# Optimization experiments

Hardware: AMD Instinct MI355X
Metric: run time of the kernel (lower is better)

The kernel has to match this reference:

```python
import jax, jax.numpy as jnp
import numpy as np

DEPTH, HEADS, DH, DIM = 12, 12, 64, 768
SPARSITY = 0.5
EPS = 1e-5


def layernorm(x, g, b):
    mu = jnp.mean(x, axis=-1, keepdims=True)
    var = jnp.var(x, axis=-1, keepdims=True)
    return (x - mu) * jax.lax.rsqrt(var + EPS) * g + b


def ternary(W, sparsity):
    # TeTRA-style ternary quantization with magnitude-based sparsity:
    # drop the `sparsity` fraction of smallest-|w| weights, remaining -> sign(w)*mean|W|.
    a = jnp.abs(W)
    thr = jnp.quantile(a.ravel(), sparsity)
    scale = jnp.mean(a)
    return jnp.where(a >= thr, jnp.sign(W) * scale, jnp.zeros_like(W))


def setup_inputs() -> dict:
    key = jax.random.key(0)
    ks = jax.random.split(key, 10)
    w = lambda k, shape: jax.random.normal(k, shape, dtype=jnp.float32) * 0.02
    return {
        "img": jax.random.normal(ks[0], (32, 3, 224, 224), dtype=jnp.float32),
        "patch_ln_g": jnp.ones((768,), jnp.float32),
        "patch_ln_b": jnp.zeros((768,), jnp.float32),
        "W_patch": w(ks[1], (768, 768)),
        "b_patch": jnp.zeros((768,), jnp.float32),
        "emb_ln_g": jnp.ones((768,), jnp.float32),
        "emb_ln_b": jnp.zeros((768,), jnp.float32),
        "pos_emb": jax.random.normal(ks[2], (1, 197, 768), dtype=jnp.float32),
        "cls_token": jax.random.normal(ks[3], (1, 1, 768), dtype=jnp.float32),
        "ln1_g": jnp.ones((DEPTH, 768), jnp.float32),
        "ln1_b": jnp.zeros((DEPTH, 768), jnp.float32),
        "Wqkv": w(ks[4], (DEPTH, 768, 3 * HEADS * DH)),
        "b_qkv": jnp.zeros((DEPTH, 3 * HEADS * DH), jnp.float32),
        "Wo": w(ks[5], (DEPTH, HEADS * DH, 768)),
        "b_o": jnp.zeros((DEPTH, 768), jnp.float32),
        "ln2_g": jnp.ones((DEPTH, 768), jnp.float32),
        "ln2_b": jnp.zeros((DEPTH, 768), jnp.float32),
        "W1": w(ks[6], (DEPTH, 768, 3072)),
        "b1": jnp.zeros((DEPTH, 3072), jnp.float32),
        "W2": w(ks[7], (DEPTH, 3072, 768)),
        "b2": jnp.zeros((DEPTH, 768), jnp.float32),
        "norm_g": jnp.ones((768,), jnp.float32),
        "norm_b": jnp.zeros((768,), jnp.float32),
    }


def reference(img, patch_ln_g, patch_ln_b, W_patch, b_patch, emb_ln_g, emb_ln_b,
              pos_emb, cls_token, ln1_g, ln1_b, Wqkv, b_qkv, Wo, b_o,
              ln2_g, ln2_b, W1, b1, W2, b2, norm_g, norm_b):
    B = img.shape[0]
    P = 16
    # b c (h p1) (w p2) -> b (h w) (p1 p2 c)
    x = img.reshape(B, 3, 14, P, 14, P).transpose(0, 2, 4, 3, 5, 1).reshape(B, 196, P * P * 3)
    x = layernorm(x, patch_ln_g, patch_ln_b)
    x = x @ W_patch + b_patch
    x = layernorm(x, emb_ln_g, emb_ln_b)
    cls = jnp.broadcast_to(cls_token, (B, 1, DIM))
    x = jnp.concatenate([cls, x], axis=1) + pos_emb  # [B, 197, 768]

    scale = DH ** -0.5
    for i in range(DEPTH):
        # sparse-ternary attention
        h = layernorm(x, ln1_g[i], ln1_b[i])
        qkv = h @ ternary(Wqkv[i], SPARSITY) + b_qkv[i]
        q, k, v = jnp.split(qkv, 3, axis=-1)
        q = q.reshape(B, -1, HEADS, DH).transpose(0, 2, 1, 3)
        k = k.reshape(B, -1, HEADS, DH).transpose(0, 2, 1, 3)
        v = v.reshape(B, -1, HEADS, DH).transpose(0, 2, 1, 3)
        attn = jax.nn.softmax(jnp.einsum('bhid,bhjd->bhij', q, k) * scale, axis=-1)
        o = jnp.einsum('bhij,bhjd->bhid', attn, v).transpose(0, 2, 1, 3).reshape(B, -1, HEADS * DH)
        x = x + (o @ ternary(Wo[i], SPARSITY) + b_o[i])
        # feed-forward (last layer uses full-precision weights)
        h = layernorm(x, ln2_g[i], ln2_b[i])
        if i < DEPTH - 1:
            W1q, W2q = ternary(W1[i], SPARSITY), ternary(W2[i], SPARSITY)
        else:
            W1q, W2q = W1[i], W2[i]
        x = x + (jax.nn.gelu(h @ W1q + b1[i]) @ W2q + b2[i])

    return layernorm(x, norm_g, norm_b)
```

## Files before the change

kernel.cpp:

```cpp
#include <hip/hip_runtime.h>

typedef unsigned short ushort_t;
typedef unsigned int uint_t;
typedef float f32x4 __attribute__((ext_vector_type(4)));
typedef short bf16x8 __attribute__((ext_vector_type(8)));

#define B_ 32
#define T_ 197
#define M_ 6304
#define M0_ 6272
#define DEPTH_ 12
#define NMAT_ 46
#define HBINS_ 16384

#define X_OFF    0ULL
#define H_OFF    19365888ULL
#define QKVB_OFF 29048832ULL
#define O_OFF    58097664ULL
#define MID_OFF  67780608ULL
#define WT_OFF   106512384ULL
#define HIST_OFF 111230976ULL
#define H2_OFF   114245632ULL
#define SUMS_OFF 120274944ULL
#define SEL_OFF  120275200ULL
#define PAR_OFF  120276224ULL

__device__ __forceinline__ float b2f(ushort_t u) {
    return __uint_as_float(((uint_t)u) << 16);
}
__device__ __forceinline__ ushort_t f2b(float f) {
    uint_t u = __float_as_uint(f);
    u += 0x7FFFu + ((u >> 16) & 1u);
    return (ushort_t)(u >> 16);
}
__device__ __forceinline__ float gelu_f(float v) {
    float u = 0.7978845608028654f * (v + 0.044715f * v * v * v);
    return v / (1.f + __expf(-2.f * u));
}

__device__ __forceinline__ void gld_lds16(void* lds, const void* g) {
    __builtin_amdgcn_global_load_lds(
        (const __attribute__((address_space(1))) unsigned int*)g,
        (__attribute__((address_space(3))) unsigned int*)lds, 16, 0, 0);
}

__device__ __forceinline__ void mat_info(int m, const float* Wqkv, const float* Wo,
                                         const float* W1, const float* W2,
                                         const float** W, int* N) {
    if (m < 12)      { *W = Wqkv + (size_t)m * 1769472;        *N = 1769472; }
    else if (m < 24) { *W = Wo   + (size_t)(m - 12) * 589824;  *N = 589824; }
    else if (m < 35) { *W = W1   + (size_t)(m - 24) * 2359296; *N = 2359296; }
    else             { *W = W2   + (size_t)(m - 35) * 2359296; *N = 2359296; }
}
__device__ __forceinline__ int mat_n(int m) {
    if (m < 12) return 1769472;
    if (m < 24) return 589824;
    return 2359296;
}

__global__ __launch_bounds__(256) void hist1_kernel(const float* Wqkv, const float* Wo,
                                                    const float* W1, const float* W2,
                                                    uint_t* hist, float* sums) {
    __shared__ uint_t lh[HBINS_];
    int m = blockIdx.y;
    const float* W; int N;
    mat_info(m, Wqkv, Wo, W1, W2, &W, &N);
    int t = threadIdx.x;
    for (int i = t; i < HBINS_; i += 256) lh[i] = 0;
    __syncthreads();
    float s = 0.f;
    const float4* W4 = (const float4*)W;
    int ntile = N >> 12;
    for (int tb = blockIdx.x; tb < ntile; tb += gridDim.x) {
        const float4* p = W4 + (size_t)tb * 1024 + t;
        float4 w0 = p[0];
        float4 w1 = p[256];
        float4 w2 = p[512];
        float4 w3 = p[768];
        float vs[16] = { w0.x, w0.y, w0.z, w0.w, w1.x, w1.y, w1.z, w1.w,
                         w2.x, w2.y, w2.z, w2.w, w3.x, w3.y, w3.z, w3.w };
        #pragma unroll
        for (int q = 0; q < 16; q++) {
            uint_t ub = __float_as_uint(vs[q]) & 0x7FFFFFFFu;
            s += __uint_as_float(ub);
            uint_t bin = ub >> 17;
            if (bin > 16383u) bin = 16383u;
            atomicAdd(&lh[bin], 1u);
        }
    }
    __syncthreads();
    uint_t* gh = hist + (size_t)m * HBINS_;
    for (int i = t; i < HBINS_; i += 256)
        if (lh[i]) atomicAdd(&gh[i], lh[i]);
    for (int off = 32; off > 0; off >>= 1) s += __shfl_down(s, off, 64);
    if ((t & 63) == 0) atomicAdd(&sums[m], s);
}

__global__ __launch_bounds__(256) void sel1_kernel(const uint_t* hist, uint_t* sel) {
    int m = blockIdx.x, t = threadIdx.x;
    const uint_t* gh = hist + (size_t)m * HBINS_;
    int N = mat_n(m);
    uint_t own = 0;
    for (int i = 0; i < 64; i++) own += gh[t * 64 + i];
    __shared__ uint_t cs[256];
    cs[t] = own; __syncthreads();
    for (int o = 1; o < 256; o <<= 1) {
        uint_t vv = (t >= o) ? cs[t - o] : 0u;
        __syncthreads();
        cs[t] += vv;
        __syncthreads();
    }
    uint_t c = cs[t] - own;
    uint_t r1 = (uint_t)(N >> 1), r2 = r1 + 1;
    for (int i = 0; i < 64; i++) {
        uint_t hv = gh[t * 64 + i];
        if (hv) {
            uint_t bin = (uint_t)(t * 64 + i);
            if (r1 > c && r1 <= c + hv) { sel[m * 4 + 0] = bin; sel[m * 4 + 1] = c; }
            if (r2 > c && r2 <= c + hv) { sel[m * 4 + 2] = bin; sel[m * 4 + 3] = c; }
            c += hv;
        }
    }
}

__global__ __launch_bounds__(256) void hist2_kernel(const float* Wqkv, const float* Wo,
                                                    const float* W1, const float* W2,
                                                    const uint_t* sel, uint_t* h2) {
    int m = blockIdx.y;
    const float* W; int N;
    mat_info(m, Wqkv, Wo, W1, W2, &W, &N);
    uint_t b1 = sel[m * 4 + 0], b2 = sel[m * 4 + 2];
    uint_t* ha = h2 + (size_t)m * 2 * HBINS_;
    uint_t* hb = ha + HBINS_;
    int t = threadIdx.x;
    const float4* W4 = (const float4*)W;
    int ntile = N >> 12;
    for (int tb = blockIdx.x; tb < ntile; tb += gridDim.x) {
        const float4* p = W4 + (size_t)tb * 1024 + t;
        float4 w0 = p[0];
        float4 w1 = p[256];
        float4 w2 = p[512];
        float4 w3 = p[768];
        float vs[16] = { w0.x, w0.y, w0.z, w0.w, w1.x, w1.y, w1.z, w1.w,
                         w2.x, w2.y, w2.z, w2.w, w3.x, w3.y, w3.z, w3.w };
        #pragma unroll
        for (int q = 0; q < 16; q++) {
            uint_t ub = __float_as_uint(vs[q]) & 0x7FFFFFFFu;
            uint_t bin = ub >> 17;
            uint_t sub = (ub >> 3) & 0x3FFFu;
            if (bin == b1) atomicAdd(&ha[sub], 1u);
            if (bin == b2 && b2 != b1) atomicAdd(&hb[sub], 1u);
        }
    }
}

__global__ __launch_bounds__(256) void sel2_kernel(const uint_t* h2, const uint_t* sel,
                                                   const float* sums, float* par) {
    int m = blockIdx.x, t = threadIdx.x;
    int N = mat_n(m);
    uint_t b1 = sel[m * 4 + 0], below1 = sel[m * 4 + 1];
    uint_t b2 = sel[m * 4 + 2], below2 = sel[m * 4 + 3];
    const uint_t* ha = h2 + (size_t)m * 2 * HBINS_;
    const uint_t* hb = (b2 == b1) ? ha : ha + HBINS_;
    uint_t r1 = (uint_t)(N >> 1) - below1;
    uint_t r2 = (uint_t)(N >> 1) + 1 - below2;
    __shared__ uint_t cs[256];
    __shared__ uint_t subs[2];
    uint_t own = 0;
    for (int i = 0; i < 64; i++) own += ha[t * 64 + i];
    cs[t] = own; __syncthreads();
    for (int o = 1; o < 256; o <<= 1) {
        uint_t vv = (t >= o) ? cs[t - o] : 0u;
        __syncthreads(); cs[t] += vv; __syncthreads();
    }
    uint_t c = cs[t] - own;
    for (int i = 0; i < 64; i++) {
        uint_t hv = ha[t * 64 + i];
        if (hv) {
            if (r1 > c && r1 <= c + hv) subs[0] = (uint_t)(t * 64 + i);
            c += hv;
        }
    }
    __syncthreads();
    own = 0;
    for (int i = 0; i < 64; i++) own += hb[t * 64 + i];
    cs[t] = own; __syncthreads();
    for (int o = 1; o < 256; o <<= 1) {
        uint_t vv = (t >= o) ? cs[t - o] : 0u;
        __syncthreads(); cs[t] += vv; __syncthreads();
    }
    c = cs[t] - own;
    for (int i = 0; i < 64; i++) {
        uint_t hv = hb[t * 64 + i];
        if (hv) {
            if (r2 > c && r2 <= c + hv) subs[1] = (uint_t)(t * 64 + i);
            c += hv;
        }
    }
    __syncthreads();
    if (t == 0) {
        float v1 = __uint_as_float((b1 << 17) | (subs[0] << 3) | 4u);
        float v2 = __uint_as_float((b2 << 17) | (subs[1] << 3) | 4u);
        par[2 * m]     = 0.5f * (v1 + v2);
        par[2 * m + 1] = sums[m] / (float)N;
    }
}

__global__ __launch_bounds__(256) void trq_kernel(const float* W, ushort_t* Wt,
                                                  int K, int N, const float* params, int pidx) {
    __shared__ ushort_t tile[32][33];
    int n0 = blockIdx.x * 32, k0 = blockIdx.y * 32;
    int t = threadIdx.x;
    float thr = 0.f; ushort_t sq = 0;
    if (pidx >= 0) {
        thr = params[2 * pidx];
        sq  = f2b(params[2 * pidx + 1]);
    }
    int c = t & 31, r0 = t >> 5;
    for (int rr = r0; rr < 32; rr += 8) {
        float w = W[(size_t)(k0 + rr) * N + n0 + c];
        ushort_t u;
        if (pidx >= 0) {
            ushort_t sgn = (ushort_t)((__float_as_uint(w) >> 16) & 0x8000u);
            u = (fabsf(w) >= thr) ? (ushort_t)(sq | sgn) : (ushort_t)0;
        } else {
            u = f2b(w);
        }
        tile[rr][c] = u;
    }
    __syncthreads();
    int kk = t & 31, nr = t >> 5;
    for (int nn = nr; nn < 32; nn += 8)
        Wt[(size_t)(n0 + nn) * K + k0 + kk] = tile[kk][nn];
}

__global__ __launch_bounds__(256) void patchify_kernel(const float* img, const float* g,
                                                       const float* b, ushort_t* A0) {
    int blk = blockIdx.x;
    int bb = blk / 196, p = blk % 196;
    int ph = p / 14, pw = p % 14;
    int t = threadIdx.x;
    float v[3];
    #pragma unroll
    for (int i = 0; i < 3; i++) {
        int d = t + i * 256;
        int c = d % 3, pix = d / 3, p2 = pix & 15, p1 = pix >> 4;
        size_t idx = (((size_t)(bb * 3 + c) * 224) + ph * 16 + p1) * 224 + pw * 16 + p2;
        v[i] = img[idx];
    }
    __shared__ float s1[256], s2[256];
    s1[t] = v[0] + v[1] + v[2];
    s2[t] = v[0] * v[0] + v[1] * v[1] + v[2] * v[2];
    __syncthreads();
    for (int o = 128; o > 0; o >>= 1) {
        if (t < o) { s1[t] += s1[t + o]; s2[t] += s2[t + o]; }
        __syncthreads();
    }
    float mu = s1[0] * (1.f / 768.f);
    float var = s2[0] * (1.f / 768.f) - mu * mu;
    float rs = rsqrtf(var + 1e-5f);
    #pragma unroll
    for (int i = 0; i < 3; i++) {
        int d = t + i * 256;
        A0[(size_t)blk * 768 + d] = f2b((v[i] - mu) * rs * g[d] + b[d]);
    }
}

__global__ __launch_bounds__(256) void assemble_kernel(const ushort_t* P, const float* cls,
                                                       const float* pos, const float* g,
                                                       const float* b, float* X) {
    int r = blockIdx.x;
    int bb = r / 197, tk = r % 197;
    int t = threadIdx.x;
    if (tk == 0) {
        #pragma unroll
        for (int i = 0; i < 3; i++) {
            int d = t + i * 256;
            X[(size_t)r * 768 + d] = cls[d] + pos[d];
        }
        return;
    }
    const ushort_t* pr = P + (size_t)(bb * 196 + tk - 1) * 768;
    float v[3];
    #pragma unroll
    for (int i = 0; i < 3; i++) v[i] = b2f(pr[t + i * 256]);
    __shared__ float s1[256], s2[256];
    s1[t] = v[0] + v[1] + v[2];
    s2[t] = v[0] * v[0] + v[1] * v[1] + v[2] * v[2];
    __syncthreads();
    for (int o = 128; o > 0; o >>= 1) {
        if (t < o) { s1[t] += s1[t + o]; s2[t] += s2[t + o]; }
        __syncthreads();
    }
    float mu = s1[0] * (1.f / 768.f);
    float var = s2[0] * (1.f / 768.f) - mu * mu;
    float rs = rsqrtf(var + 1e-5f);
    #pragma unroll
    for (int i = 0; i < 3; i++) {
        int d = t + i * 256;
        X[(size_t)r * 768 + d] =
            (v[i] - mu) * rs * g[d] + b[d] + pos[(size_t)tk * 768 + d];
    }
}

__global__ __launch_bounds__(256) void ln_kernel(const float* X, ushort_t* Hb, float* Hf,
                                                 const float* g, const float* b) {
    int r = blockIdx.x, t = threadIdx.x;
    const float* xr = X + (size_t)r * 768;
    float v0 = xr[t], v1 = xr[t + 256], v2 = xr[t + 512];
    __shared__ float s1[256], s2[256];
    s1[t] = v0 + v1 + v2;
    s2[t] = v0 * v0 + v1 * v1 + v2 * v2;
    __syncthreads();
    for (int o = 128; o > 0; o >>= 1) {
        if (t < o) { s1[t] += s1[t + o]; s2[t] += s2[t + o]; }
        __syncthreads();
    }
    float mu = s1[0] * (1.f / 768.f);
    float var = s2[0] * (1.f / 768.f) - mu * mu;
    float rs = rsqrtf(var + 1e-5f);
    float o0 = (v0 - mu) * rs * g[t]       + b[t];
    float o1 = (v1 - mu) * rs * g[t + 256] + b[t + 256];
    float o2 = (v2 - mu) * rs * g[t + 512] + b[t + 512];
    if (Hf) {
        Hf[(size_t)r * 768 + t] = o0;
        Hf[(size_t)r * 768 + t + 256] = o1;
        Hf[(size_t)r * 768 + t + 512] = o2;
    } else {
        Hb[(size_t)r * 768 + t] = f2b(o0);
        Hb[(size_t)r * 768 + t + 256] = f2b(o1);
        Hb[(size_t)r * 768 + t + 512] = f2b(o2);
    }
}

__global__ __launch_bounds__(256) void gemm_kernel(const ushort_t* A, const ushort_t* Bt,
                                                   const float* bias, void* Cout,
                                                   const float* R, int M, int N, int K, int epi) {
    __shared__ ushort_t As[128 * 32];
    __shared__ ushort_t Bs[128 * 32];
    int t = threadIdx.x;
    int lane = t & 63, wave = t >> 6;
    int row0 = blockIdx.y * 128, col0 = blockIdx.x * 128;
    int wm = (wave >> 1) * 64, wn = (wave & 1) * 64;
    int fr = lane & 15, fq = lane >> 4;

    int srow = t >> 2;
    int scol = (t & 3) * 8;
    const ushort_t* gA0 = A + (size_t)min(row0 + srow, M - 1) * K + scol;
    const ushort_t* gA1 = A + (size_t)min(row0 + 64 + srow, M - 1) * K + scol;
    const ushort_t* gB0 = Bt + (size_t)(col0 + srow) * K + scol;
    const ushort_t* gB1 = Bt + (size_t)(col0 + 64 + srow) * K + scol;
    ushort_t* lA0 = &As[t * 8];
    ushort_t* lA1 = &As[2048 + t * 8];
    ushort_t* lB0 = &Bs[t * 8];
    ushort_t* lB1 = &Bs[2048 + t * 8];

    f32x4 acc[4][4];
    #pragma unroll
    for (int i = 0; i < 4; i++)
        #pragma unroll
        for (int j = 0; j < 4; j++)
            acc[i][j] = (f32x4){0.f, 0.f, 0.f, 0.f};

    for (int k0 = 0; k0 < K; k0 += 32) {
        gld_lds16(lA0, gA0 + k0);
        gld_lds16(lA1, gA1 + k0);
        gld_lds16(lB0, gB0 + k0);
        gld_lds16(lB1, gB1 + k0);
        __syncthreads();
        bf16x8 af[4], bfr[4];
        #pragma unroll
        for (int mt = 0; mt < 4; mt++)
            af[mt] = *(const bf16x8*)&As[(wm + mt * 16 + fr) * 32 + fq * 8];
        #pragma unroll
        for (int nt = 0; nt < 4; nt++)
            bfr[nt] = *(const bf16x8*)&Bs[(wn + nt * 16 + fr) * 32 + fq * 8];
        #pragma unroll
        for (int mt = 0; mt < 4; mt++)
            #pragma unroll
            for (int nt = 0; nt < 4; nt++)
                acc[mt][nt] = __builtin_amdgcn_mfma_f32_16x16x32_bf16(
                    af[mt], bfr[nt], acc[mt][nt], 0, 0, 0);
        __syncthreads();
    }
    #pragma unroll
    for (int nt = 0; nt < 4; nt++) {
        int col = col0 + wn + nt * 16 + fr;
        float bv = bias[col];
        #pragma unroll
        for (int mt = 0; mt < 4; mt++) {
            #pragma unroll
            for (int gi = 0; gi < 4; gi++) {
                int row = row0 + wm + mt * 16 + fq * 4 + gi;
                if (row < M) {
                    float val = acc[mt][nt][gi] + bv;
                    if (epi == 1) val = gelu_f(val);
                    size_t off = (size_t)row * N + col;
                    if (epi == 2) ((float*)Cout)[off] = val + R[off];
                    else          ((ushort_t*)Cout)[off] = f2b(val);
                }
            }
        }
    }
}

#define TPAD_ 224
#define KROW_ 72
#define VROW_ 232
__global__ __launch_bounds__(256) void attn_kernel(const ushort_t* qkv, ushort_t* O) {
    __shared__ ushort_t KbP[TPAD_ * KROW_];
    __shared__ ushort_t Vt[64 * VROW_];
    int qt = blockIdx.x;
    int bh = blockIdx.y;
    int bb = bh / 12, hh = bh % 12;
    int t = threadIdx.x, lane = t & 63, w = t >> 6;
    int q = lane >> 4, n = lane & 15;
    size_t base = (size_t)bb * 197 * 2304 + hh * 64;

    for (int e = t; e < TPAD_ * 8; e += 256) {
        int j = e >> 3, d8 = e & 7;
        uint4 kv = make_uint4(0u, 0u, 0u, 0u);
        if (j < 197) kv = *(const uint4*)(qkv + base + (size_t)j * 2304 + 768 + d8 * 8);
        *(uint4*)&KbP[j * KROW_ + d8 * 8] = kv;
    }
    for (int d8 = 0; d8 < 8; d8++) {
        int j = t;
        if (j < 197) {
            uint4 vv = *(const uint4*)(qkv + base + (size_t)j * 2304 + 1536 + d8 * 8);
            ushort_t tmp[8];
            *(uint4*)tmp = vv;
            #pragma unroll
            for (int i = 0; i < 8; i++) Vt[(d8 * 8 + i) * VROW_ + j] = tmp[i];
        }
    }
    {
        int j = 197 + (t & 31);
        if (j < TPAD_)
            for (int d = t >> 5; d < 64; d += 8) Vt[d * VROW_ + j] = 0;
    }
    __syncthreads();

    int i0 = qt * 64 + w * 16;
    bf16x8 qf[2];
    {
        int row = i0 + n;
        #pragma unroll
        for (int kc = 0; kc < 2; kc++) {
            uint4 qv = make_uint4(0u, 0u, 0u, 0u);
            if (row < 197)
                qv = *(const uint4*)(qkv + base + (size_t)row * 2304 + kc * 32 + q * 8);
            qf[kc] = *(bf16x8*)&qv;
        }
    }
    f32x4 sa[14];
    #pragma unroll
    for (int ct = 0; ct < 14; ct++) sa[ct] = (f32x4){0.f, 0.f, 0.f, 0.f};
    #pragma unroll
    for (int kc = 0; kc < 2; kc++) {
        #pragma unroll
        for (int ct = 0; ct < 14; ct++) {
            bf16x8 kf = *(const bf16x8*)&KbP[(ct * 16 + n) * KROW_ + kc * 32 + q * 8];
            sa[ct] = __builtin_amdgcn_mfma_f32_16x16x32_bf16(qf[kc], kf, sa[ct], 0, 0, 0);
        }
    }
    float mx[4] = {-1e30f, -1e30f, -1e30f, -1e30f};
    #pragma unroll
    for (int ct = 0; ct < 14; ct++) {
        bool v = (ct * 16 + n) < 197;
        #pragma unroll
        for (int gi = 0; gi < 4; gi++) {
            float s = sa[ct][gi] * 0.125f;
            sa[ct][gi] = s;
            if (v) mx[gi] = fmaxf(mx[gi], s);
        }
    }
    #pragma unroll
    for (int msk = 1; msk < 16; msk <<= 1)
        #pragma unroll
        for (int gi = 0; gi < 4; gi++)
            mx[gi] = fmaxf(mx[gi], __shfl_xor(mx[gi], msk, 64));
    float sm[4] = {0.f, 0.f, 0.f, 0.f};
    #pragma unroll
    for (int ct = 0; ct < 14; ct++) {
        bool v = (ct * 16 + n) < 197;
        #pragma unroll
        for (int gi = 0; gi < 4; gi++) {
            float p = v ? __expf(sa[ct][gi] - mx[gi]) : 0.f;
            sa[ct][gi] = p;
            sm[gi] += p;
        }
    }
    #pragma unroll
    for (int msk = 1; msk < 16; msk <<= 1)
        #pragma unroll
        for (int gi = 0; gi < 4; gi++)
            sm[gi] += __shfl_xor(sm[gi], msk, 64);
    #pragma unroll
    for (int gi = 0; gi < 4; gi++) sm[gi] = 1.f / sm[gi];

    __syncthreads();

    #pragma unroll
    for (int ct = 0; ct < 14; ct++)
        #pragma unroll
        for (int gi = 0; gi < 4; gi++)
            KbP[(w * 16 + q * 4 + gi) * VROW_ + ct * 16 + n] = f2b(sa[ct][gi] * sm[gi]);

    f32x4 oa[4];
    #pragma unroll
    for (int nt = 0; nt < 4; nt++) oa[nt] = (f32x4){0.f, 0.f, 0.f, 0.f};
    #pragma unroll
    for (int kc = 0; kc < 7; kc++) {
        bf16x8 pf = *(const bf16x8*)&KbP[(w * 16 + n) * VROW_ + kc * 32 + q * 8];
        #pragma unroll
        for (int nt = 0; nt < 4; nt++) {
            bf16x8 vf = *(const bf16x8*)&Vt[(nt * 16 + n) * VROW_ + kc * 32 + q * 8];
            oa[nt] = __builtin_amdgcn_mfma_f32_16x16x32_bf16(pf, vf, oa[nt], 0, 0, 0);
        }
    }
    #pragma unroll
    for (int nt = 0; nt < 4; nt++) {
        #pragma unroll
        for (int gi = 0; gi < 4; gi++) {
            int row = i0 + q * 4 + gi;
            if (row < 197)
                O[((size_t)bb * 197 + row) * 768 + hh * 64 + nt * 16 + n] = f2b(oa[nt][gi]);
        }
    }
}

extern "C" void kernel_launch(void* const* d_in, const int* in_sizes, int n_in,
                              void* d_out, int out_size, void* d_ws, size_t ws_size,
                              hipStream_t stream) {
    const float* img   = (const float*)d_in[0];
    const float* plg   = (const float*)d_in[1];
    const float* plb   = (const float*)d_in[2];
    const float* Wp    = (const float*)d_in[3];
    const float* bp    = (const float*)d_in[4];
    const float* elg   = (const float*)d_in[5];
    const float* elb   = (const float*)d_in[6];
    const float* pos   = (const float*)d_in[7];
    const float* cls   = (const float*)d_in[8];
    const float* l1g   = (const float*)d_in[9];
    const float* l1b   = (const float*)d_in[10];
    const float* Wqkv  = (const float*)d_in[11];
    const float* bqkv  = (const float*)d_in[12];
    const float* Wo    = (const float*)d_in[13];
    const float* bo    = (const float*)d_in[14];
    const float* l2g   = (const float*)d_in[15];
    const float* l2b   = (const float*)d_in[16];
    const float* W1    = (const float*)d_in[17];
    const float* b1    = (const float*)d_in[18];
    const float* W2    = (const float*)d_in[19];
    const float* b2    = (const float*)d_in[20];
    const float* ng    = (const float*)d_in[21];
    const float* nb    = (const float*)d_in[22];

    char* ws = (char*)d_ws;
    float*    x    = (float*)(ws + X_OFF);
    ushort_t* h    = (ushort_t*)(ws + H_OFF);
    ushort_t* qkvb = (ushort_t*)(ws + QKVB_OFF);
    ushort_t* o    = (ushort_t*)(ws + O_OFF);
    ushort_t* mid  = (ushort_t*)(ws + MID_OFF);
    ushort_t* wt   = (ushort_t*)(ws + WT_OFF);
    uint_t*   hist = (uint_t*)(ws + HIST_OFF);
    uint_t*   h2   = (uint_t*)(ws + H2_OFF);
    float*    sums = (float*)(ws + SUMS_OFF);
    uint_t*   sel  = (uint_t*)(ws + SEL_OFF);
    float*    par  = (float*)(ws + PAR_OFF);

    hipMemsetAsync(ws + HIST_OFF, 0, SEL_OFF - HIST_OFF, stream);

    hist1_kernel<<<dim3(64, NMAT_), 256, 0, stream>>>(Wqkv, Wo, W1, W2, hist, sums);
    sel1_kernel<<<NMAT_, 256, 0, stream>>>(hist, sel);
    hist2_kernel<<<dim3(64, NMAT_), 256, 0, stream>>>(Wqkv, Wo, W1, W2, sel, h2);
    sel2_kernel<<<NMAT_, 256, 0, stream>>>(h2, sel, sums, par);

    patchify_kernel<<<M0_, 256, 0, stream>>>(img, plg, plb, h);
    trq_kernel<<<dim3(768 / 32, 768 / 32), 256, 0, stream>>>(Wp, wt, 768, 768, par, -1);
    gemm_kernel<<<dim3(6, 49), 256, 0, stream>>>(h, wt, bp, o, nullptr, M0_, 768, 768, 0);
    assemble_kernel<<<M_, 256, 0, stream>>>(o, cls, pos, elg, elb, x);

    for (int i = 0; i < DEPTH_; i++) {
        ln_kernel<<<M_, 256, 0, stream>>>(x, h, nullptr, l1g + i * 768, l1b + i * 768);
        trq_kernel<<<dim3(2304 / 32, 768 / 32), 256, 0, stream>>>(
            Wqkv + (size_t)i * 1769472, wt, 768, 2304, par, i);
        gemm_kernel<<<dim3(18, 50), 256, 0, stream>>>(h, wt, bqkv + i * 2304, qkvb, nullptr,
                                                      M_, 2304, 768, 0);
        attn_kernel<<<dim3(4, B_ * 12), 256, 0, stream>>>(qkvb, o);
        trq_kernel<<<dim3(768 / 32, 768 / 32), 256, 0, stream>>>(
            Wo + (size_t)i * 589824, wt, 768, 768, par, 12 + i);
        gemm_kernel<<<dim3(6, 50), 256, 0, stream>>>(o, wt, bo + i * 768, x, x,
                                                     M_, 768, 768, 2);
        ln_kernel<<<M_, 256, 0, stream>>>(x, h, nullptr, l2g + i * 768, l2b + i * 768);
        trq_kernel<<<dim3(3072 / 32, 768 / 32), 256, 0, stream>>>(
            W1 + (size_t)i * 2359296, wt, 768, 3072, par, (i < 11) ? 24 + i : -1);
        gemm_kernel<<<dim3(24, 50), 256, 0, stream>>>(h, wt, b1 + i * 3072, mid, nullptr,
                                                      M_, 3072, 768, 1);
        trq_kernel<<<dim3(768 / 32, 3072 / 32), 256, 0, stream>>>(
            W2 + (size_t)i * 2359296, wt, 3072, 768, par, (i < 11) ? 35 + i : -1);
        gemm_kernel<<<dim3(6, 50), 256, 0, stream>>>(mid, wt, b2 + i * 768, x, x,
                                                     M_, 768, 3072, 2);
    }

    ln_kernel<<<M_, 256, 0, stream>>>(x, nullptr, (float*)d_out, ng, nb);
}
```

Measured before the change: 4.807 ms.

## Double-buffer GEMM LDS, add narrow-tile variant, prefetch and pack histogram

The GEMM now double-buffers its A/B shared-memory tiles so the next K-slice's global-to-LDS loads are issued before the MFMAs on the current slice, leaving one barrier per step. It is templated on tile width, and the three N=768 GEMMs use 64-wide tiles so twice as many blocks fill the GPU. The histogram kernels prefetch the next weight tile into registers while binning the current one. hist1 also packs two 16-bit counters per 32-bit shared word, halving LDS use, at the risk of a per-block counter overflowing 65535 and with the clamp for bins above 16383 removed.

```diff
diff --git a/kernel.cpp b/kernel.cpp
--- a/kernel.cpp
+++ b/kernel.cpp
@@ -61,37 +61,48 @@
 __global__ __launch_bounds__(256) void hist1_kernel(const float* Wqkv, const float* Wo,
                                                     const float* W1, const float* W2,
                                                     uint_t* hist, float* sums) {
-    __shared__ uint_t lh[HBINS_];
+    __shared__ uint_t lh[HBINS_ / 2];
     int m = blockIdx.y;
     const float* W; int N;
     mat_info(m, Wqkv, Wo, W1, W2, &W, &N);
     int t = threadIdx.x;
-    for (int i = t; i < HBINS_; i += 256) lh[i] = 0;
+    for (int i = t; i < HBINS_ / 2; i += 256) lh[i] = 0;
     __syncthreads();
     float s = 0.f;
     const float4* W4 = (const float4*)W;
     int ntile = N >> 12;
-    for (int tb = blockIdx.x; tb < ntile; tb += gridDim.x) {
+    int tb = blockIdx.x;
+    float4 c0 = {}, c1 = {}, c2 = {}, c3 = {};
+    if (tb < ntile) {
         const float4* p = W4 + (size_t)tb * 1024 + t;
-        float4 w0 = p[0];
-        float4 w1 = p[256];
-        float4 w2 = p[512];
-        float4 w3 = p[768];
-        float vs[16] = { w0.x, w0.y, w0.z, w0.w, w1.x, w1.y, w1.z, w1.w,
-                         w2.x, w2.y, w2.z, w2.w, w3.x, w3.y, w3.z, w3.w };
+        c0 = p[0]; c1 = p[256]; c2 = p[512]; c3 = p[768];
+    }
+    while (tb < ntile) {
+        int nx = tb + gridDim.x;
+        float4 n0 = {}, n1 = {}, n2 = {}, n3 = {};
+        if (nx < ntile) {
+            const float4* p = W4 + (size_t)nx * 1024 + t;
+            n0 = p[0]; n1 = p[256]; n2 = p[512]; n3 = p[768];
+        }
+        float vs[16] = { c0.x, c0.y, c0.z, c0.w, c1.x, c1.y, c1.z, c1.w,
+                         c2.x, c2.y, c2.z, c2.w, c3.x, c3.y, c3.z, c3.w };
         #pragma unroll
         for (int q = 0; q < 16; q++) {
             uint_t ub = __float_as_uint(vs[q]) & 0x7FFFFFFFu;
             s += __uint_as_float(ub);
             uint_t bin = ub >> 17;
-            if (bin > 16383u) bin = 16383u;
-            atomicAdd(&lh[bin], 1u);
-        }
+            atomicAdd(&lh[bin >> 1], 1u << ((bin & 1u) << 4));
+        }
+        c0 = n0; c1 = n1; c2 = n2; c3 = n3;
+        tb = nx;
     }
     __syncthreads();
     uint_t* gh = hist + (size_t)m * HBINS_;
-    for (int i = t; i < HBINS_; i += 256)
-        if (lh[i]) atomicAdd(&gh[i], lh[i]);
+    for (int i = t; i < HBINS_ / 2; i += 256) {
+        uint_t v = lh[i];
+        if (v & 0xFFFFu) atomicAdd(&gh[2 * i], v & 0xFFFFu);
+        if (v >> 16)     atomicAdd(&gh[2 * i + 1], v >> 16);
+    }
     for (int off = 32; off > 0; off >>= 1) s += __shfl_down(s, off, 64);
     if ((t & 63) == 0) atomicAdd(&sums[m], s);
 }
@@ -135,14 +146,21 @@
     int t = threadIdx.x;
     const float4* W4 = (const float4*)W;
     int ntile = N >> 12;
-    for (int tb = blockIdx.x; tb < ntile; tb += gridDim.x) {
+    int tb = blockIdx.x;
+    float4 c0 = {}, c1 = {}, c2 = {}, c3 = {};
+    if (tb < ntile) {
         const float4* p = W4 + (size_t)tb * 1024 + t;
-        float4 w0 = p[0];
-        float4 w1 = p[256];
-        float4 w2 = p[512];
-        float4 w3 = p[768];
-        float vs[16] = { w0.x, w0.y, w0.z, w0.w, w1.x, w1.y, w1.z, w1.w,
-                         w2.x, w2.y, w2.z, w2.w, w3.x, w3.y, w3.z, w3.w };
+        c0 = p[0]; c1 = p[256]; c2 = p[512]; c3 = p[768];
+    }
+    while (tb < ntile) {
+        int nx = tb + gridDim.x;
+        float4 n0 = {}, n1 = {}, n2 = {}, n3 = {};
+        if (nx < ntile) {
+            const float4* p = W4 + (size_t)nx * 1024 + t;
+            n0 = p[0]; n1 = p[256]; n2 = p[512]; n3 = p[768];
+        }
+        float vs[16] = { c0.x, c0.y, c0.z, c0.w, c1.x, c1.y, c1.z, c1.w,
+                         c2.x, c2.y, c2.z, c2.w, c3.x, c3.y, c3.z, c3.w };
         #pragma unroll
         for (int q = 0; q < 16; q++) {
             uint_t ub = __float_as_uint(vs[q]) & 0x7FFFFFFFu;
@@ -151,6 +169,8 @@
             if (bin == b1) atomicAdd(&ha[sub], 1u);
             if (bin == b2 && b2 != b1) atomicAdd(&hb[sub], 1u);
         }
+        c0 = n0; c1 = n1; c2 = n2; c3 = n3;
+        tb = nx;
     }
 }
 
@@ -333,15 +353,17 @@
     }
 }
 
+template<int BN>
 __global__ __launch_bounds__(256) void gemm_kernel(const ushort_t* A, const ushort_t* Bt,
                                                    const float* bias, void* Cout,
                                                    const float* R, int M, int N, int K, int epi) {
-    __shared__ ushort_t As[128 * 32];
-    __shared__ ushort_t Bs[128 * 32];
+    constexpr int NT = BN / 32;
+    __shared__ ushort_t As[2][128 * 32];
+    __shared__ ushort_t Bs[2][BN * 32];
     int t = threadIdx.x;
     int lane = t & 63, wave = t >> 6;
-    int row0 = blockIdx.y * 128, col0 = blockIdx.x * 128;
-    int wm = (wave >> 1) * 64, wn = (wave & 1) * 64;
+    int row0 = blockIdx.y * 128, col0 = blockIdx.x * BN;
+    int wm = (wave >> 1) * 64, wn = (wave & 1) * (BN / 2);
     int fr = lane & 15, fq = lane >> 4;
 
     int srow = t >> 2;
@@ -349,42 +371,49 @@
     const ushort_t* gA0 = A + (size_t)min(row0 + srow, M - 1) * K + scol;
     const ushort_t* gA1 = A + (size_t)min(row0 + 64 + srow, M - 1) * K + scol;
     const ushort_t* gB0 = Bt + (size_t)(col0 + srow) * K + scol;
-    const ushort_t* gB1 = Bt + (size_t)(col0 + 64 + srow) * K + scol;
-    ushort_t* lA0 = &As[t * 8];
-    ushort_t* lA1 = &As[2048 + t * 8];
-    ushort_t* lB0 = &Bs[t * 8];
-    ushort_t* lB1 = &Bs[2048 + t * 8];
-
-    f32x4 acc[4][4];
+    const ushort_t* gB1 = (BN == 128)
+        ? Bt + (size_t)(col0 + 64 + srow) * K + scol : gB0;
+
+    f32x4 acc[4][NT];
     #pragma unroll
     for (int i = 0; i < 4; i++)
         #pragma unroll
-        for (int j = 0; j < 4; j++)
+        for (int j = 0; j < NT; j++)
             acc[i][j] = (f32x4){0.f, 0.f, 0.f, 0.f};
 
+    gld_lds16(&As[0][t * 8], gA0);
+    gld_lds16(&As[0][2048 + t * 8], gA1);
+    gld_lds16(&Bs[0][t * 8], gB0);
+    if (BN == 128) gld_lds16(&Bs[0][2048 + t * 8], gB1);
+    __syncthreads();
+
+    int cur = 0;
     for (int k0 = 0; k0 < K; k0 += 32) {
-        gld_lds16(lA0, gA0 + k0);
-        gld_lds16(lA1, gA1 + k0);
-        gld_lds16(lB0, gB0 + k0);
-        gld_lds16(lB1, gB1 + k0);
-        __syncthreads();
-        bf16x8 af[4], bfr[4];
+        int kn = k0 + 32;
+        if (kn < K) {
+            gld_lds16(&As[cur ^ 1][t * 8], gA0 + kn);
+            gld_lds16(&As[cur ^ 1][2048 + t * 8], gA1 + kn);
+            gld_lds16(&Bs[cur ^ 1][t * 8], gB0 + kn);
+            if (BN == 128) gld_lds16(&Bs[cur ^ 1][2048 + t * 8], gB1 + kn);
+        }
+        bf16x8 af[4], bfr[NT];
         #pragma unroll
         for (int mt = 0; mt < 4; mt++)
-            af[mt] = *(const bf16x8*)&As[(wm + mt * 16 + fr) * 32 + fq * 8];
-        #pragma unroll
-        for (int nt = 0; nt < 4; nt++)
-            bfr[nt] = *(const bf16x8*)&Bs[(wn + nt * 16 + fr) * 32 + fq * 8];
+            af[mt] = *(const bf16x8*)&As[cur][(wm + mt * 16 + fr) * 32 + fq * 8];
+        #pragma unroll
+        for (int nt = 0; nt < NT; nt++)
+            bfr[nt] = *(const bf16x8*)&Bs[cur][(wn + nt * 16 + fr) * 32 + fq * 8];
         #pragma unroll
         for (int mt = 0; mt < 4; mt++)
             #pragma unroll
-            for (int nt = 0; nt < 4; nt++)
+            for (int nt = 0; nt < NT; nt++)
                 acc[mt][nt] = __builtin_amdgcn_mfma_f32_16x16x32_bf16(
                     af[mt], bfr[nt], acc[mt][nt], 0, 0, 0);
         __syncthreads();
-    }
-    #pragma unroll
-    for (int nt = 0; nt < 4; nt++) {
+        cur ^= 1;
+    }
+    #pragma unroll
+    for (int nt = 0; nt < NT; nt++) {
         int col = col0 + wn + nt * 16 + fr;
         float bv = bias[col];
         #pragma unroll
@@ -578,29 +607,29 @@
 
     patchify_kernel<<<M0_, 256, 0, stream>>>(img, plg, plb, h);
     trq_kernel<<<dim3(768 / 32, 768 / 32), 256, 0, stream>>>(Wp, wt, 768, 768, par, -1);
-    gemm_kernel<<<dim3(6, 49), 256, 0, stream>>>(h, wt, bp, o, nullptr, M0_, 768, 768, 0);
+    gemm_kernel<64><<<dim3(12, 49), 256, 0, stream>>>(h, wt, bp, o, nullptr, M0_, 768, 768, 0);
     assemble_kernel<<<M_, 256, 0, stream>>>(o, cls, pos, elg, elb, x);
 
     for (int i = 0; i < DEPTH_; i++) {
         ln_kernel<<<M_, 256, 0, stream>>>(x, h, nullptr, l1g + i * 768, l1b + i * 768);
         trq_kernel<<<dim3(2304 / 32, 768 / 32), 256, 0, stream>>>(
             Wqkv + (size_t)i * 1769472, wt, 768, 2304, par, i);
-        gemm_kernel<<<dim3(18, 50), 256, 0, stream>>>(h, wt, bqkv + i * 2304, qkvb, nullptr,
-                                                      M_, 2304, 768, 0);
+        gemm_kernel<128><<<dim3(18, 50), 256, 0, stream>>>(h, wt, bqkv + i * 2304, qkvb,
+                                                           nullptr, M_, 2304, 768, 0);
         attn_kernel<<<dim3(4, B_ * 12), 256, 0, stream>>>(qkvb, o);
         trq_kernel<<<dim3(768 / 32, 768 / 32), 256, 0, stream>>>(
             Wo + (size_t)i * 589824, wt, 768, 768, par, 12 + i);
-        gemm_kernel<<<dim3(6, 50), 256, 0, stream>>>(o, wt, bo + i * 768, x, x,
-                                                     M_, 768, 768, 2);
+        gemm_kernel<64><<<dim3(12, 50), 256, 0, stream>>>(o, wt, bo + i * 768, x, x,
+                                                          M_, 768, 768, 2);
         ln_kernel<<<M_, 256, 0, stream>>>(x, h, nullptr, l2g + i * 768, l2b + i * 768);
         trq_kernel<<<dim3(3072 / 32, 768 / 32), 256, 0, stream>>>(
             W1 + (size_t)i * 2359296, wt, 768, 3072, par, (i < 11) ? 24 + i : -1);
-        gemm_kernel<<<dim3(24, 50), 256, 0, stream>>>(h, wt, b1 + i * 3072, mid, nullptr,
-                                                      M_, 3072, 768, 1);
+        gemm_kernel<128><<<dim3(24, 50), 256, 0, stream>>>(h, wt, b1 + i * 3072, mid,
+                                                           nullptr, M_, 3072, 768, 1);
         trq_kernel<<<dim3(768 / 32, 3072 / 32), 256, 0, stream>>>(
             W2 + (size_t)i * 2359296, wt, 3072, 768, par, (i < 11) ? 35 + i : -1);
-        gemm_kernel<<<dim3(6, 50), 256, 0, stream>>>(mid, wt, b2 + i * 768, x, x,
-                                                     M_, 768, 3072, 2);
+        gemm_kernel<64><<<dim3(12, 50), 256, 0, stream>>>(mid, wt, b2 + i * 768, x, x,
+                                                          M_, 768, 3072, 2);
     }
 
     ln_kernel<<<M_, 256, 0, stream>>>(x, nullptr, (float*)d_out, ng, nb);
```

Measured after the change: 4.275 ms. -11.1%, faster.
